# Kernel tuning notes

Hardware: AMD Instinct MI355X
Metric: run time of the kernel (lower is better)

Reference implementation:

```python
import jax, jax.numpy as jnp
import numpy as np

N_NODES = 50000
D_FEAT = 128
HIDDEN = 256
CLASSES = 40
N_EDGES = 800000


def setup_inputs() -> dict:
    key = jax.random.key(0)
    ks = jax.random.split(key, 8)
    x = jax.random.normal(ks[0], (N_NODES, D_FEAT), dtype=jnp.float32)
    edge_index = jax.random.randint(ks[1], (2, N_EDGES), 0, N_NODES, dtype=jnp.int64)
    s1 = 1.0 / np.sqrt(D_FEAT)
    s2 = 1.0 / np.sqrt(HIDDEN)
    # PyG SAGEConv: lin_l (applied to aggregated neighbors, has bias), lin_r (root, no bias)
    Wl1 = jax.random.uniform(ks[2], (HIDDEN, D_FEAT), jnp.float32, -s1, s1)
    bl1 = jnp.zeros((HIDDEN,), jnp.float32)
    Wr1 = jax.random.uniform(ks[3], (HIDDEN, D_FEAT), jnp.float32, -s1, s1)
    Wl2 = jax.random.uniform(ks[4], (CLASSES, HIDDEN), jnp.float32, -s2, s2)
    bl2 = jnp.zeros((CLASSES,), jnp.float32)
    Wr2 = jax.random.uniform(ks[5], (CLASSES, HIDDEN), jnp.float32, -s2, s2)
    return {"x": x, "edge_index": edge_index, "Wl1": Wl1, "bl1": bl1, "Wr1": Wr1,
            "Wl2": Wl2, "bl2": bl2, "Wr2": Wr2}


def _mean_aggregate(x, src, dst, n_nodes):
    # gather source features along edges, scatter-mean into destinations
    summed = jax.ops.segment_sum(x[src], dst, num_segments=n_nodes)  # [N, d]
    counts = jax.ops.segment_sum(jnp.ones((src.shape[0],), x.dtype), dst,
                                 num_segments=n_nodes)
    return summed / jnp.maximum(counts, 1.0)[:, None]


def _sage_conv(x, src, dst, Wl, bl, Wr):
    agg = _mean_aggregate(x, src, dst, x.shape[0])
    return agg @ Wl.T + bl + x @ Wr.T


def reference(x, edge_index, Wl1, bl1, Wr1, Wl2, bl2, Wr2):
    src, dst = edge_index[0], edge_index[1]
    h = _sage_conv(x, src, dst, Wl1, bl1, Wr1)
    h = jax.nn.relu(h)
    # F.dropout(training=self.training): eval-mode inference -> identity
    h = _sage_conv(h, src, dst, Wl2, bl2, Wr2)
    return jax.nn.log_softmax(h, axis=1)
```

## Files before the change

kernel.cpp:

```cpp
#include <hip/hip_runtime.h>
#include <hip/hip_bf16.h>
#include <math.h>

#define N_NODES 50000
#define D_FEAT  128
#define HIDDEN  256
#define CLASSES 40
#define N_EDGES 800000
#define P2S 64
#define R2S 48
#define SCAN_NB 196
#define HLS 264
#define ALS 136
#define NTILES 3125
#define GRID_L 512
#define NBUCK 196
#define BCAP  5120
#define BA_BLOCKS 784

typedef unsigned int  u32;
typedef unsigned short u16;
typedef __attribute__((ext_vector_type(8))) short short8;
typedef __attribute__((ext_vector_type(4))) float floatx4;

__device__ __forceinline__ float bf_lo(u32 w) { union { u32 i; float f; } u; u.i = w << 16; return u.f; }
__device__ __forceinline__ float bf_hi(u32 w) { union { u32 i; float f; } u; u.i = w & 0xffff0000u; return u.f; }
__device__ __forceinline__ float bf1(u16 h)   { union { u32 i; float f; } u; u.i = ((u32)h) << 16; return u.f; }
__device__ __forceinline__ u16 f2bf(float f) {
  union { float f; u32 i; } u; u.f = f; u32 i = u.i;
  return (u16)((i + 0x7fffu + ((i >> 16) & 1u)) >> 16);
}
__device__ __forceinline__ u32 packbf(float a, float b) { return (u32)f2bf(a) | ((u32)f2bf(b) << 16); }

__device__ __forceinline__ bool edges_are_i64(const void* eraw) {
  const long long* p = (const long long*)eraw;
  bool ok = true;
  #pragma unroll
  for (int i = 0; i < 8; i++) {
    long long v = p[(size_t)i * 100003];
    ok = ok && (v >= 0) && (v < N_NODES);
  }
  return ok;
}

__global__ __launch_bounds__(256) void bucketA_kernel(
    const void* __restrict__ eraw, int* __restrict__ bcur, u32* __restrict__ bbuf) {
  __shared__ int hist[NBUCK], base[NBUCK], loc[NBUCK];
  const bool i64f = edges_are_i64(eraw);
  const int t = threadIdx.x;
  for (int i = t; i < NBUCK; i += 256) { hist[i] = 0; loc[i] = 0; }
  __syncthreads();

  int sreg[4], dreg[4];
  const int e0 = blockIdx.x * 1024;
  #pragma unroll
  for (int j = 0; j < 4; j++) {
    int e = e0 + j * 256 + t;
    int ss = 0, dd = -1;
    if (e < N_EDGES) {
      if (i64f) {
        const long long* p = (const long long*)eraw;
        ss = (int)p[e]; dd = (int)p[N_EDGES + e];
      } else {
        const int* p = (const int*)eraw;
        ss = p[e]; dd = p[N_EDGES + e];
      }
      if ((u32)ss >= N_NODES || (u32)dd >= N_NODES) dd = -1;
    }
    sreg[j] = ss; dreg[j] = dd;
    if (dd >= 0) atomicAdd(&hist[dd >> 8], 1);
  }
  __syncthreads();
  for (int i = t; i < NBUCK; i += 256)
    base[i] = atomicAdd(&bcur[i], hist[i]);
  __syncthreads();
  #pragma unroll
  for (int j = 0; j < 4; j++) {
    int dd = dreg[j];
    if (dd >= 0) {
      int bk = dd >> 8;
      int pos = base[bk] + atomicAdd(&loc[bk], 1);
      if (pos < BCAP)
        bbuf[(size_t)bk * BCAP + pos] = (u32)sreg[j] | ((u32)(dd & 255) << 16);
    }
  }
}

__global__ __launch_bounds__(256) void bscan_kernel(
    const u32* __restrict__ bbuf, const int* __restrict__ bcur,
    int* __restrict__ offsets, int* __restrict__ blocksums) {
  __shared__ int cnt[256];
  __shared__ int lds[256];
  const int t = threadIdx.x;
  const int b = blockIdx.x;
  cnt[t] = 0;
  __syncthreads();
  const int n = min(bcur[b], BCAP);
  for (int i = t; i < n; i += 256) {
    u32 e = bbuf[(size_t)b * BCAP + i];
    atomicAdd(&cnt[(e >> 16) & 255], 1);
  }
  __syncthreads();
  int c = cnt[t];
  lds[t] = c;
  __syncthreads();
  #pragma unroll
  for (int d = 1; d < 256; d <<= 1) {
    int v = (t >= d) ? lds[t - d] : 0;
    __syncthreads();
    lds[t] += v;
    __syncthreads();
  }
  offsets[b * 256 + t] = lds[t] - c;
  if (t == 255) blocksums[b] = lds[255];
}

__global__ __launch_bounds__(256) void scan2_kernel(
    const int* __restrict__ blocksums, int* __restrict__ btops,
    int* __restrict__ offsets) {
  __shared__ int lds[256];
  const int t = threadIdx.x;
  int c = (t < SCAN_NB) ? blocksums[t] : 0;
  lds[t] = c;
  __syncthreads();
  #pragma unroll
  for (int d = 1; d < 256; d <<= 1) {
    int v = (t >= d) ? lds[t - d] : 0;
    __syncthreads();
    lds[t] += v;
    __syncthreads();
  }
  if (t < SCAN_NB) btops[t] = lds[t] - c;
  if (t == SCAN_NB - 1) offsets[N_NODES] = lds[t];
}

__global__ __launch_bounds__(256) void bucketB_kernel(
    const u32* __restrict__ bbuf, const int* __restrict__ bcur,
    const int* __restrict__ btops, int* __restrict__ offsets,
    int* __restrict__ csr) {
  __shared__ int cur[256];
  const int t = threadIdx.x;
  const int b = blockIdx.x;
  const int node = b * 256 + t;
  int off = 0;
  if (node < N_NODES) {
    off = offsets[node] + btops[b];
    offsets[node] = off;
  }
  cur[t] = off;
  __syncthreads();
  const int n = min(bcur[b], BCAP);
  for (int i = t; i < n; i += 256) {
    u32 e = bbuf[(size_t)b * BCAP + i];
    int dl = (e >> 16) & 255;
    int pos = atomicAdd(&cur[dl], 1);
    csr[pos] = (int)(e & 0xFFFFu);
  }
}

__global__ __launch_bounds__(256) void cvt_all_kernel(
    const float* __restrict__ x,
    const float* __restrict__ Wl1, const float* __restrict__ Wr1,
    const float* __restrict__ Wl2, const float* __restrict__ Wr2,
    u16* __restrict__ xb, u16* __restrict__ wb, int* __restrict__ bcur) {
  if (blockIdx.x < 6250) {
    int i = (blockIdx.x * 256 + threadIdx.x) * 4;
    float4 v = *(const float4*)(x + i);
    u32* o = (u32*)(xb + i);
    o[0] = packbf(v.x, v.y);
    o[1] = packbf(v.z, v.w);
  } else {
    if (blockIdx.x == 6250 && threadIdx.x < NBUCK) bcur[threadIdx.x] = 0;
    int i = (blockIdx.x - 6250) * 256 + threadIdx.x;
    if (i < 32768)      wb[i] = f2bf(Wl1[i]);
    else if (i < 65536) wb[i] = f2bf(Wr1[i - 32768]);
    else if (i < 75776) wb[i] = f2bf(Wl2[i - 65536]);
    else if (i < 86016) wb[i] = f2bf(Wr2[i - 75776]);
  }
}

__global__ __launch_bounds__(256) void gather1_kernel(
    const u16* __restrict__ xb, const int* __restrict__ offsets,
    const int* __restrict__ csr_src, u16* __restrict__ agg1) {
  const int node = blockIdx.x * 4 + (threadIdx.x >> 6);
  const int lane = threadIdx.x & 63;
  int b = offsets[node], e = offsets[node + 1];
  float a0 = 0.f, a1 = 0.f, b0 = 0.f, b1 = 0.f;
  float c0 = 0.f, c1 = 0.f, d0 = 0.f, d1 = 0.f;
  float e0 = 0.f, e1 = 0.f, f0 = 0.f, f1 = 0.f;
  float g0 = 0.f, g1 = 0.f, h0 = 0.f, h1 = 0.f;
  int i = b;
  for (; i + 8 <= e; i += 8) {
    int s0 = csr_src[i],     s1 = csr_src[i + 1], s2 = csr_src[i + 2], s3 = csr_src[i + 3];
    int s4 = csr_src[i + 4], s5 = csr_src[i + 5], s6 = csr_src[i + 6], s7 = csr_src[i + 7];
    u32 w0 = ((const u32*)(xb + (size_t)s0 * D_FEAT))[lane];
    u32 w1 = ((const u32*)(xb + (size_t)s1 * D_FEAT))[lane];
    u32 w2 = ((const u32*)(xb + (size_t)s2 * D_FEAT))[lane];
    u32 w3 = ((const u32*)(xb + (size_t)s3 * D_FEAT))[lane];
    u32 w4 = ((const u32*)(xb + (size_t)s4 * D_FEAT))[lane];
    u32 w5 = ((const u32*)(xb + (size_t)s5 * D_FEAT))[lane];
    u32 w6 = ((const u32*)(xb + (size_t)s6 * D_FEAT))[lane];
    u32 w7 = ((const u32*)(xb + (size_t)s7 * D_FEAT))[lane];
    a0 += bf_lo(w0); a1 += bf_hi(w0);
    b0 += bf_lo(w1); b1 += bf_hi(w1);
    c0 += bf_lo(w2); c1 += bf_hi(w2);
    d0 += bf_lo(w3); d1 += bf_hi(w3);
    e0 += bf_lo(w4); e1 += bf_hi(w4);
    f0 += bf_lo(w5); f1 += bf_hi(w5);
    g0 += bf_lo(w6); g1 += bf_hi(w6);
    h0 += bf_lo(w7); h1 += bf_hi(w7);
  }
  for (; i < e; i++) {
    int s = csr_src[i];
    u32 w = ((const u32*)(xb + (size_t)s * D_FEAT))[lane];
    a0 += bf_lo(w); a1 += bf_hi(w);
  }
  float s0 = ((a0 + b0) + (c0 + d0)) + ((e0 + f0) + (g0 + h0));
  float s1 = ((a1 + b1) + (c1 + d1)) + ((e1 + f1) + (g1 + h1));
  float inv = 1.0f / (float)max(e - b, 1);
  ((u32*)(agg1 + (size_t)node * D_FEAT))[lane] = packbf(s0 * inv, s1 * inv);
}

__global__ __launch_bounds__(256, 2) void layer_kernel(
    const u16* __restrict__ agg1, const u16* __restrict__ xb,
    const u16* __restrict__ Wl1b, const u16* __restrict__ Wr1b,
    const float* __restrict__ bl1,
    const u16* __restrict__ Wl2b, const u16* __restrict__ Wr2b,
    const float* __restrict__ bl2,
    u16* __restrict__ p2b, float* __restrict__ r2f) {
  __shared__ u16 h_lds[16 * HLS];
  __shared__ u16 a_lds[16 * ALS];
  __shared__ u16 x_lds[16 * ALS];
  const int lane = threadIdx.x & 63;
  const int wave = threadIdx.x >> 6;
  const int n15  = lane & 15;
  const int quad = lane >> 4;
  const int ko   = quad * 8;
  const int colbase = wave * 64;
  const int srow = (wave << 2) + quad;
  const int scol = n15 * 8;

  short8 Bf[8][4];
  #pragma unroll
  for (int s = 0; s < 8; s++) {
    const u16* W = (s < 4) ? Wl1b : Wr1b;
    const int kk = (s & 3) * 32;
    #pragma unroll
    for (int t = 0; t < 4; t++)
      Bf[s][t] = *(const short8*)(W + (size_t)(colbase + t * 16 + n15) * D_FEAT + ko + kk);
  }

  const int  c0   = wave;
  const bool isR0 = (c0 >= 3);
  const int  tc0  = c0 - (isR0 ? 3 : 0);
  const int  wr0  = min(tc0 * 16 + n15, CLASSES - 1);
  const u16* Wc0  = (isR0 ? Wr2b : Wl2b) + (size_t)wr0 * HIDDEN + ko;
  const bool has1 = (wave < 2);
  const int  tc1  = wave + 1;
  const int  wr1  = min(tc1 * 16 + n15, CLASSES - 1);
  const u16* Wc1  = Wr2b + (size_t)wr1 * HIDDEN + ko;

  const float bias0 = bl2[min(tc0 * 16 + n15, CLASSES - 1)];
  const float bias1 = bl2[min(tc1 * 16 + n15, CLASSES - 1)];

  for (int tile = blockIdx.x; tile < NTILES; tile += GRID_L) {
    const int m0 = tile * 16;
    {
      const size_t g = (size_t)(m0 + srow) * D_FEAT + scol;
      *(short8*)(a_lds + srow * ALS + scol) = *(const short8*)(agg1 + g);
      *(short8*)(x_lds + srow * ALS + scol) = *(const short8*)(xb + g);
    }
    __syncthreads();
    {
      floatx4 acc[4];
      #pragma unroll
      for (int t = 0; t < 4; t++) acc[t] = floatx4{0.f, 0.f, 0.f, 0.f};

      short8 a[4];
      #pragma unroll
      for (int s = 0; s < 4; s++) a[s] = *(const short8*)(a_lds + n15 * ALS + ko + s * 32);
      #pragma unroll
      for (int s = 0; s < 4; s++)
        #pragma unroll
        for (int t = 0; t < 4; t++)
          acc[t] = __builtin_amdgcn_mfma_f32_16x16x32_bf16(a[s], Bf[s][t], acc[t], 0, 0, 0);
      #pragma unroll
      for (int s = 0; s < 4; s++) a[s] = *(const short8*)(x_lds + n15 * ALS + ko + s * 32);
      #pragma unroll
      for (int s = 0; s < 4; s++)
        #pragma unroll
        for (int t = 0; t < 4; t++)
          acc[t] = __builtin_amdgcn_mfma_f32_16x16x32_bf16(a[s], Bf[4 + s][t], acc[t], 0, 0, 0);

      #pragma unroll
      for (int t = 0; t < 4; t++) {
        int col = colbase + t * 16 + n15;
        float bias = bl1[col];
        #pragma unroll
        for (int r = 0; r < 4; r++) {
          float v = acc[t][r] + bias;
          v = v > 0.f ? v : 0.f;
          h_lds[(quad * 4 + r) * HLS + col] = f2bf(v);
        }
      }
    }
    __syncthreads();
    {
      floatx4 acc0 = floatx4{0.f, 0.f, 0.f, 0.f};
      floatx4 acc1 = floatx4{0.f, 0.f, 0.f, 0.f};
      #pragma unroll
      for (int s = 0; s < 8; s++) {
        short8 a2 = *(const short8*)(&h_lds[n15 * HLS + s * 32 + ko]);
        acc0 = __builtin_amdgcn_mfma_f32_16x16x32_bf16(a2, *(const short8*)(Wc0 + s * 32), acc0, 0, 0, 0);
        if (has1)
          acc1 = __builtin_amdgcn_mfma_f32_16x16x32_bf16(a2, *(const short8*)(Wc1 + s * 32), acc1, 0, 0, 0);
      }
      {
        int col = tc0 * 16 + n15;
        #pragma unroll
        for (int r = 0; r < 4; r++) {
          int row = m0 + quad * 4 + r;
          if (isR0) r2f[(size_t)row * R2S + col] = acc0[r] + bias0;
          else      p2b[(size_t)row * P2S + col] = f2bf(acc0[r]);
        }
      }
      if (has1) {
        int col = tc1 * 16 + n15;
        #pragma unroll
        for (int r = 0; r < 4; r++) {
          int row = m0 + quad * 4 + r;
          r2f[(size_t)row * R2S + col] = acc1[r] + bias1;
        }
      }
    }
    __syncthreads();
  }
}

__global__ __launch_bounds__(256) void final_kernel(
    const u16* __restrict__ p2b, const float* __restrict__ r2f,
    const int* __restrict__ offsets, const int* __restrict__ csr_src,
    float* __restrict__ out) {
  const int node = blockIdx.x * 4 + (threadIdx.x >> 6);
  const int lane = threadIdx.x & 63;
  int b = offsets[node], e = offsets[node + 1];
  float s[16];
  #pragma unroll
  for (int j = 0; j < 16; j++) s[j] = 0.f;
  int i = b;
  for (; i + 16 <= e; i += 16) {
    int c[16];
    #pragma unroll
    for (int j = 0; j < 16; j++) c[j] = csr_src[i + j];
    #pragma unroll
    for (int j = 0; j < 16; j++) s[j] += bf1(p2b[(size_t)c[j] * P2S + lane]);
  }
  for (; i + 8 <= e; i += 8) {
    int c[8];
    #pragma unroll
    for (int j = 0; j < 8; j++) c[j] = csr_src[i + j];
    #pragma unroll
    for (int j = 0; j < 8; j++) s[j] += bf1(p2b[(size_t)c[j] * P2S + lane]);
  }
  for (; i < e; i++) {
    int sc = csr_src[i];
    s[0] += bf1(p2b[(size_t)sc * P2S + lane]);
  }
  float sum4[4];
  #pragma unroll
  for (int j = 0; j < 4; j++)
    sum4[j] = (s[j] + s[j + 4]) + (s[j + 8] + s[j + 12]);
  float ssum = (sum4[0] + sum4[1]) + (sum4[2] + sum4[3]);
  float inv = 1.0f / (float)max(e - b, 1);
  const bool act = (lane < CLASSES);
  float v = act ? (ssum * inv + r2f[(size_t)node * R2S + lane]) : -INFINITY;
  float mx = v;
  #pragma unroll
  for (int d = 1; d < 64; d <<= 1) mx = fmaxf(mx, __shfl_xor(mx, d, 64));
  float ex = act ? expf(v - mx) : 0.f;
  float sum = ex;
  #pragma unroll
  for (int d = 1; d < 64; d <<= 1) sum += __shfl_xor(sum, d, 64);
  float l = mx + logf(sum);
  if (act) out[(size_t)node * CLASSES + lane] = v - l;
}

extern "C" void kernel_launch(void* const* d_in, const int* in_sizes, int n_in,
                              void* d_out, int out_size, void* d_ws, size_t ws_size,
                              hipStream_t stream) {
  const float* x   = (const float*)d_in[0];
  const void*  ei  = d_in[1];
  const float* Wl1 = (const float*)d_in[2];
  const float* bl1 = (const float*)d_in[3];
  const float* Wr1 = (const float*)d_in[4];
  const float* Wl2 = (const float*)d_in[5];
  const float* bl2 = (const float*)d_in[6];
  const float* Wr2 = (const float*)d_in[7];

  char* ws = (char*)d_ws;
  size_t off = 0;
  int* csr       = (int*)(ws + off); off += (size_t)N_EDGES * 4;
  int* offsets   = (int*)(ws + off); off += 204800;
  int* blocksums = (int*)(ws + off); off += 1024;
  int* btops     = (int*)(ws + off); off += 1024;
  int* bcur      = (int*)(ws + off); off += 1024;
  u32* bbuf      = (u32*)(ws + off); off += (size_t)NBUCK * BCAP * 4;
  u16* wb        = (u16*)(ws + off); off += 172288;
  u16* xb        = (u16*)(ws + off); off += (size_t)N_NODES * D_FEAT * 2;
  u16* agg1      = (u16*)(ws + off); off += (size_t)N_NODES * D_FEAT * 2;
  u16* p2b       = (u16*)(ws + off); off += (size_t)N_NODES * P2S * 2;
  float* r2f     = (float*)(ws + off); off += (size_t)N_NODES * R2S * 4;

  u16* Wl1b = wb;
  u16* Wr1b = wb + 32768;
  u16* Wl2b = wb + 65536;
  u16* Wr2b = wb + 75776;

  cvt_all_kernel<<<6250 + 336, 256, 0, stream>>>(x, Wl1, Wr1, Wl2, Wr2, xb, wb, bcur);
  bucketA_kernel<<<BA_BLOCKS, 256, 0, stream>>>(ei, bcur, bbuf);
  bscan_kernel<<<NBUCK, 256, 0, stream>>>(bbuf, bcur, offsets, blocksums);
  scan2_kernel<<<1, 256, 0, stream>>>(blocksums, btops, offsets);
  bucketB_kernel<<<NBUCK, 256, 0, stream>>>(bbuf, bcur, btops, offsets, csr);
  gather1_kernel<<<N_NODES / 4, 256, 0, stream>>>(xb, offsets, csr, agg1);
  layer_kernel<<<GRID_L, 256, 0, stream>>>(agg1, xb, Wl1b, Wr1b, bl1,
                                           Wl2b, Wr2b, bl2, p2b, r2f);
  final_kernel<<<N_NODES / 4, 256, 0, stream>>>(p2b, r2f, offsets, csr, (float*)d_out);
}
```

Measured before the change: 228.7 us.

## Fuse CSR scan kernels and split layer-2 projection buffer into compact arrays

Merges the bucket scan, global scan and scatter kernels into one kernel, with each block redundantly scanning the 196 bucket counts, which removes two launches and the blocksums/btops round trips. Moves the weight conversion into extra blocks of the bucketing kernel. Splits the padded 64-wide bf16 layer-2 projection into a 32-wide array and an 8-wide array, so the final gather reads 80 bytes per neighbor instead of a 128-byte padded row. In exchange, the two gather reads per edge now target separate arrays, and every scatter block repeats the small scan.

```diff
diff --git a/kernel.cpp b/kernel.cpp
--- a/kernel.cpp
+++ b/kernel.cpp
@@ -7,9 +7,7 @@
 #define HIDDEN  256
 #define CLASSES 40
 #define N_EDGES 800000
-#define P2S 64
 #define R2S 48
-#define SCAN_NB 196
 #define HLS 264
 #define ALS 136
 #define NTILES 3125
@@ -17,6 +15,7 @@
 #define NBUCK 196
 #define BCAP  5120
 #define BA_BLOCKS 784
+#define WCVT_BLOCKS 336
 
 typedef unsigned int  u32;
 typedef unsigned short u16;
@@ -43,8 +42,32 @@
   return ok;
 }
 
+__global__ __launch_bounds__(256) void cvt_x_kernel(
+    const float* __restrict__ x, u16* __restrict__ xb, int* __restrict__ bcur) {
+  if (blockIdx.x < 6250) {
+    int i = (blockIdx.x * 256 + threadIdx.x) * 4;
+    float4 v = *(const float4*)(x + i);
+    u32* o = (u32*)(xb + i);
+    o[0] = packbf(v.x, v.y);
+    o[1] = packbf(v.z, v.w);
+  } else {
+    if (threadIdx.x < NBUCK) bcur[threadIdx.x] = 0;
+  }
+}
+
 __global__ __launch_bounds__(256) void bucketA_kernel(
-    const void* __restrict__ eraw, int* __restrict__ bcur, u32* __restrict__ bbuf) {
+    const void* __restrict__ eraw, int* __restrict__ bcur, u32* __restrict__ bbuf,
+    const float* __restrict__ Wl1, const float* __restrict__ Wr1,
+    const float* __restrict__ Wl2, const float* __restrict__ Wr2,
+    u16* __restrict__ wb) {
+  if (blockIdx.x >= BA_BLOCKS) {
+    int i = (blockIdx.x - BA_BLOCKS) * 256 + threadIdx.x;
+    if (i < 32768)      wb[i] = f2bf(Wl1[i]);
+    else if (i < 65536) wb[i] = f2bf(Wr1[i - 32768]);
+    else if (i < 75776) wb[i] = f2bf(Wl2[i - 65536]);
+    else if (i < 86016) wb[i] = f2bf(Wr2[i - 75776]);
+    return;
+  }
   __shared__ int hist[NBUCK], base[NBUCK], loc[NBUCK];
   const bool i64f = edges_are_i64(eraw);
   const int t = threadIdx.x;
@@ -86,13 +109,25 @@
   }
 }
 
-__global__ __launch_bounds__(256) void bscan_kernel(
+__global__ __launch_bounds__(256) void bucketBC_kernel(
     const u32* __restrict__ bbuf, const int* __restrict__ bcur,
-    int* __restrict__ offsets, int* __restrict__ blocksums) {
+    int* __restrict__ offsets, int* __restrict__ csr) {
   __shared__ int cnt[256];
   __shared__ int lds[256];
   const int t = threadIdx.x;
   const int b = blockIdx.x;
+  int c196 = (t < NBUCK) ? min(bcur[t], BCAP) : 0;
+  lds[t] = c196;
+  __syncthreads();
+  #pragma unroll
+  for (int d = 1; d < 256; d <<= 1) {
+    int v = (t >= d) ? lds[t - d] : 0;
+    __syncthreads();
+    lds[t] += v;
+    __syncthreads();
+  }
+  const int btop = (b > 0) ? lds[b - 1] : 0;
+  if (b == NBUCK - 1 && t == 0) offsets[N_NODES] = lds[NBUCK - 1];
   cnt[t] = 0;
   __syncthreads();
   const int n = min(bcur[b], BCAP);
@@ -111,71 +146,16 @@
     lds[t] += v;
     __syncthreads();
   }
-  offsets[b * 256 + t] = lds[t] - c;
-  if (t == 255) blocksums[b] = lds[255];
-}
-
-__global__ __launch_bounds__(256) void scan2_kernel(
-    const int* __restrict__ blocksums, int* __restrict__ btops,
-    int* __restrict__ offsets) {
-  __shared__ int lds[256];
-  const int t = threadIdx.x;
-  int c = (t < SCAN_NB) ? blocksums[t] : 0;
-  lds[t] = c;
-  __syncthreads();
-  #pragma unroll
-  for (int d = 1; d < 256; d <<= 1) {
-    int v = (t >= d) ? lds[t - d] : 0;
-    __syncthreads();
-    lds[t] += v;
-    __syncthreads();
-  }
-  if (t < SCAN_NB) btops[t] = lds[t] - c;
-  if (t == SCAN_NB - 1) offsets[N_NODES] = lds[t];
-}
-
-__global__ __launch_bounds__(256) void bucketB_kernel(
-    const u32* __restrict__ bbuf, const int* __restrict__ bcur,
-    const int* __restrict__ btops, int* __restrict__ offsets,
-    int* __restrict__ csr) {
-  __shared__ int cur[256];
-  const int t = threadIdx.x;
-  const int b = blockIdx.x;
   const int node = b * 256 + t;
-  int off = 0;
-  if (node < N_NODES) {
-    off = offsets[node] + btops[b];
-    offsets[node] = off;
-  }
-  cur[t] = off;
-  __syncthreads();
-  const int n = min(bcur[b], BCAP);
+  const int off = lds[t] - c + btop;
+  if (node < N_NODES) offsets[node] = off;
+  cnt[t] = off;
+  __syncthreads();
   for (int i = t; i < n; i += 256) {
     u32 e = bbuf[(size_t)b * BCAP + i];
     int dl = (e >> 16) & 255;
-    int pos = atomicAdd(&cur[dl], 1);
+    int pos = atomicAdd(&cnt[dl], 1);
     csr[pos] = (int)(e & 0xFFFFu);
-  }
-}
-
-__global__ __launch_bounds__(256) void cvt_all_kernel(
-    const float* __restrict__ x,
-    const float* __restrict__ Wl1, const float* __restrict__ Wr1,
-    const float* __restrict__ Wl2, const float* __restrict__ Wr2,
-    u16* __restrict__ xb, u16* __restrict__ wb, int* __restrict__ bcur) {
-  if (blockIdx.x < 6250) {
-    int i = (blockIdx.x * 256 + threadIdx.x) * 4;
-    float4 v = *(const float4*)(x + i);
-    u32* o = (u32*)(xb + i);
-    o[0] = packbf(v.x, v.y);
-    o[1] = packbf(v.z, v.w);
-  } else {
-    if (blockIdx.x == 6250 && threadIdx.x < NBUCK) bcur[threadIdx.x] = 0;
-    int i = (blockIdx.x - 6250) * 256 + threadIdx.x;
-    if (i < 32768)      wb[i] = f2bf(Wl1[i]);
-    else if (i < 65536) wb[i] = f2bf(Wr1[i - 32768]);
-    else if (i < 75776) wb[i] = f2bf(Wl2[i - 65536]);
-    else if (i < 86016) wb[i] = f2bf(Wr2[i - 75776]);
   }
 }
 
@@ -227,7 +207,7 @@
     const float* __restrict__ bl1,
     const u16* __restrict__ Wl2b, const u16* __restrict__ Wr2b,
     const float* __restrict__ bl2,
-    u16* __restrict__ p2b, float* __restrict__ r2f) {
+    u16* __restrict__ p2a, u16* __restrict__ p2c, float* __restrict__ r2f) {
   __shared__ u16 h_lds[16 * HLS];
   __shared__ u16 a_lds[16 * ALS];
   __shared__ u16 x_lds[16 * ALS];
@@ -320,8 +300,13 @@
         #pragma unroll
         for (int r = 0; r < 4; r++) {
           int row = m0 + quad * 4 + r;
-          if (isR0) r2f[(size_t)row * R2S + col] = acc0[r] + bias0;
-          else      p2b[(size_t)row * P2S + col] = f2bf(acc0[r]);
+          if (isR0) {
+            r2f[(size_t)row * R2S + col] = acc0[r] + bias0;
+          } else if (col < 32) {
+            p2a[(size_t)row * 32 + col] = f2bf(acc0[r]);
+          } else if (col < CLASSES) {
+            p2c[(size_t)row * 8 + (col - 32)] = f2bf(acc0[r]);
+          }
         }
       }
       if (has1) {
@@ -338,11 +323,14 @@
 }
 
 __global__ __launch_bounds__(256) void final_kernel(
-    const u16* __restrict__ p2b, const float* __restrict__ r2f,
+    const u16* __restrict__ p2a, const u16* __restrict__ p2c,
+    const float* __restrict__ r2f,
     const int* __restrict__ offsets, const int* __restrict__ csr_src,
     float* __restrict__ out) {
   const int node = blockIdx.x * 4 + (threadIdx.x >> 6);
   const int lane = threadIdx.x & 63;
+  const u16* gb = (lane < 32) ? (p2a + lane) : (p2c + min(lane - 32, 7));
+  const int  gs = (lane < 32) ? 32 : 8;
   int b = offsets[node], e = offsets[node + 1];
   float s[16];
   #pragma unroll
@@ -353,18 +341,18 @@
     #pragma unroll
     for (int j = 0; j < 16; j++) c[j] = csr_src[i + j];
     #pragma unroll
-    for (int j = 0; j < 16; j++) s[j] += bf1(p2b[(size_t)c[j] * P2S + lane]);
+    for (int j = 0; j < 16; j++) s[j] += bf1(gb[(size_t)c[j] * gs]);
   }
   for (; i + 8 <= e; i += 8) {
     int c[8];
     #pragma unroll
     for (int j = 0; j < 8; j++) c[j] = csr_src[i + j];
     #pragma unroll
-    for (int j = 0; j < 8; j++) s[j] += bf1(p2b[(size_t)c[j] * P2S + lane]);
+    for (int j = 0; j < 8; j++) s[j] += bf1(gb[(size_t)c[j] * gs]);
   }
   for (; i < e; i++) {
     int sc = csr_src[i];
-    s[0] += bf1(p2b[(size_t)sc * P2S + lane]);
+    s[0] += bf1(gb[(size_t)sc * gs]);
   }
   float sum4[4];
   #pragma unroll
@@ -401,14 +389,13 @@
   size_t off = 0;
   int* csr       = (int*)(ws + off); off += (size_t)N_EDGES * 4;
   int* offsets   = (int*)(ws + off); off += 204800;
-  int* blocksums = (int*)(ws + off); off += 1024;
-  int* btops     = (int*)(ws + off); off += 1024;
   int* bcur      = (int*)(ws + off); off += 1024;
   u32* bbuf      = (u32*)(ws + off); off += (size_t)NBUCK * BCAP * 4;
   u16* wb        = (u16*)(ws + off); off += 172288;
   u16* xb        = (u16*)(ws + off); off += (size_t)N_NODES * D_FEAT * 2;
   u16* agg1      = (u16*)(ws + off); off += (size_t)N_NODES * D_FEAT * 2;
-  u16* p2b       = (u16*)(ws + off); off += (size_t)N_NODES * P2S * 2;
+  u16* p2a       = (u16*)(ws + off); off += (size_t)N_NODES * 32 * 2;
+  u16* p2c       = (u16*)(ws + off); off += (size_t)N_NODES * 8 * 2;
   float* r2f     = (float*)(ws + off); off += (size_t)N_NODES * R2S * 4;
 
   u16* Wl1b = wb;
@@ -416,13 +403,12 @@
   u16* Wl2b = wb + 65536;
   u16* Wr2b = wb + 75776;
 
-  cvt_all_kernel<<<6250 + 336, 256, 0, stream>>>(x, Wl1, Wr1, Wl2, Wr2, xb, wb, bcur);
-  bucketA_kernel<<<BA_BLOCKS, 256, 0, stream>>>(ei, bcur, bbuf);
-  bscan_kernel<<<NBUCK, 256, 0, stream>>>(bbuf, bcur, offsets, blocksums);
-  scan2_kernel<<<1, 256, 0, stream>>>(blocksums, btops, offsets);
-  bucketB_kernel<<<NBUCK, 256, 0, stream>>>(bbuf, bcur, btops, offsets, csr);
+  cvt_x_kernel<<<6251, 256, 0, stream>>>(x, xb, bcur);
+  bucketA_kernel<<<BA_BLOCKS + WCVT_BLOCKS, 256, 0, stream>>>(
+      ei, bcur, bbuf, Wl1, Wr1, Wl2, Wr2, wb);
+  bucketBC_kernel<<<NBUCK, 256, 0, stream>>>(bbuf, bcur, offsets, csr);
   gather1_kernel<<<N_NODES / 4, 256, 0, stream>>>(xb, offsets, csr, agg1);
   layer_kernel<<<GRID_L, 256, 0, stream>>>(agg1, xb, Wl1b, Wr1b, bl1,
-                                           Wl2b, Wr2b, bl2, p2b, r2f);
-  final_kernel<<<N_NODES / 4, 256, 0, stream>>>(p2b, r2f, offsets, csr, (float*)d_out);
-}
+                                           Wl2b, Wr2b, bl2, p2a, p2c, r2f);
+  final_kernel<<<N_NODES / 4, 256, 0, stream>>>(p2a, p2c, r2f, offsets, csr, (float*)d_out);
+}
```

After: 225.4 us. About the same (-1.4%).
